# Optimization experiments

Hardware: AMD Instinct MI355X
Metric: run time of the kernel (lower is better)

## Reference

```python
import jax, jax.numpy as jnp
import numpy as np

ROT = 256  # Hadamard block size (ConvLinear4bit._n)


def _hadamard(n):
    # Sylvester construction of the n x n Hadamard matrix (n power of 2)
    H = np.array([[1.0]], dtype=np.float32)
    while H.shape[0] < n:
        H = np.block([[H, H], [H, -H]])
    return jnp.asarray(H / np.sqrt(n), dtype=jnp.float32)


def setup_inputs() -> dict:
    key = jax.random.key(0)
    k1, k2, k3, k4 = jax.random.split(key, 4)
    N, D_in, D_out = 4096, 4096, 4096
    x = jax.random.normal(k1, (N, D_in), dtype=jnp.float32)
    # unpacked int4 weights in [-7, 7] (logical content of the packed uint8 buffer)
    weight_int = jax.random.randint(k2, (D_out, D_in), -7, 8, dtype=jnp.int32)
    # per-output-row weight scales (quarot: max|W_rot| / 7)
    w_scale = jax.random.uniform(k3, (D_out, 1), dtype=jnp.float32) * 0.01 + 1e-4
    bias = jax.random.normal(k4, (D_out,), dtype=jnp.float32) * 0.01
    return {"x": x, "weight_int": weight_int, "w_scale": w_scale, "bias": bias}


def reference(x, weight_int, w_scale, bias):
    N, D = x.shape
    H = _hadamard(ROT)
    # blockwise Hadamard rotation along the feature dim (D is a multiple of ROT)
    x_rot = (x.reshape(N, D // ROT, ROT) @ H).reshape(N, D)
    # per-row symmetric int4 quantization of activations
    scales_x = jnp.max(jnp.abs(x_rot), axis=-1, keepdims=True) / 7.0  # [N, 1]
    q_x = jnp.clip(jnp.round(x_rot / scales_x), -8, 7).astype(jnp.int32)
    acc = jnp.matmul(q_x, weight_int.T)
    # sym_dequant: row scale (activations) * col scale (weights), then bias
    out = acc.astype(jnp.float32) * scales_x * w_scale.T + bias
    return out
```

## Files before the change

### kernel.cpp

```cpp
#include <hip/hip_runtime.h>
#include <math.h>

typedef int v4i  __attribute__((ext_vector_type(4)));
typedef int v16i __attribute__((ext_vector_type(16)));

#define DIM 4096
#define BM 256
#define BK 64
#define ATILE (BM * BK)
#define BUFSZ (2 * ATILE)

__device__ __forceinline__ void async16(const void* g, void* l) {
    __builtin_amdgcn_global_load_lds((__attribute__((address_space(1))) void*)(g),
                                     (__attribute__((address_space(3))) void*)(l),
                                     16, 0, 0);
}

#define VMCNT(N) asm volatile("s_waitcnt vmcnt(" #N ")" ::: "memory")
#define BARRIER() asm volatile("s_barrier" ::: "memory")

__device__ __forceinline__ int swzC(int r) {
    return ((r >> 1) & 3) ^ ((r >> 3) & 3);
}

__global__ __launch_bounds__(256) void prep(const float* __restrict__ x,
                                            const int* __restrict__ w,
                                            signed char* __restrict__ q,
                                            signed char* __restrict__ w8,
                                            float* __restrict__ scales) {
    if (blockIdx.x >= 4096) {
        int i = (blockIdx.x - 4096) * 256 + threadIdx.x;
        int4 v = ((const int4*)w)[i];
        char4 c;
        c.x = (signed char)v.x; c.y = (signed char)v.y;
        c.z = (signed char)v.z; c.w = (signed char)v.w;
        ((char4*)w8)[i] = c;
        return;
    }
    const int row  = blockIdx.x;
    const int lane = threadIdx.x & 63;
    const int wave = threadIdx.x >> 6;
    const float4* xr4 = (const float4*)(x + (size_t)row * DIM);

    float sgn[6];
    #pragma unroll
    for (int i = 0; i < 6; ++i) sgn[i] = (lane & (1 << i)) ? -1.0f : 1.0f;

    float f[4][4];
    #pragma unroll
    for (int b = 0; b < 4; ++b) {
        const int blk = wave + 4 * b;
        float4 v = xr4[blk * 64 + lane];
        float t0 = v.x + v.y, t1 = v.x - v.y;
        float t2 = v.z + v.w, t3 = v.z - v.w;
        f[b][0] = t0 + t2; f[b][1] = t1 + t3;
        f[b][2] = t0 - t2; f[b][3] = t1 - t3;
        #pragma unroll
        for (int st = 0; st < 6; ++st) {
            const int m = 1 << st;
            #pragma unroll
            for (int j = 0; j < 4; ++j) {
                float p = __shfl_xor(f[b][j], m, 64);
                f[b][j] = fmaf(sgn[st], f[b][j], p);
            }
        }
        #pragma unroll
        for (int j = 0; j < 4; ++j) f[b][j] *= 0.0625f;
    }

    float m = 0.0f;
    #pragma unroll
    for (int b = 0; b < 4; ++b)
        #pragma unroll
        for (int j = 0; j < 4; ++j) m = fmaxf(m, fabsf(f[b][j]));
    #pragma unroll
    for (int d = 32; d; d >>= 1) m = fmaxf(m, __shfl_xor(m, d, 64));
    __shared__ float sm[4];
    if (lane == 0) sm[wave] = m;
    __syncthreads();
    m = fmaxf(fmaxf(sm[0], sm[1]), fmaxf(sm[2], sm[3]));

    const float s = m / 7.0f;
    if (threadIdx.x == 0) scales[row] = s;

    char4* qr4 = (char4*)(q + (size_t)row * DIM);
    #pragma unroll
    for (int b = 0; b < 4; ++b) {
        const int blk = wave + 4 * b;
        char4 c;
        int qi;
        qi = (int)rintf(f[b][0] / s); c.x = (signed char)min(7, max(-8, qi));
        qi = (int)rintf(f[b][1] / s); c.y = (signed char)min(7, max(-8, qi));
        qi = (int)rintf(f[b][2] / s); c.z = (signed char)min(7, max(-8, qi));
        qi = (int)rintf(f[b][3] / s); c.w = (signed char)min(7, max(-8, qi));
        qr4[blk * 64 + lane] = c;
    }
}

__global__ __launch_bounds__(512, 2) void gemm_q8(const signed char* __restrict__ A,
                                                  const signed char* __restrict__ B,
                                                  const float* __restrict__ rowScale,
                                                  const float* __restrict__ wscale,
                                                  const float* __restrict__ bias,
                                                  float* __restrict__ out) {
    __shared__ __align__(16) signed char S[4 * BUFSZ];

    const int flat = blockIdx.y * gridDim.x + blockIdx.x;
    const int xcd  = flat & 7;
    const int idx  = flat >> 3;
    const int bm   = ((xcd >> 1) << 2) + (idx & 3);
    const int bn   = ((xcd & 1) << 3) + (idx >> 2);

    const int t = threadIdx.x;
    const int lane = t & 63;
    const int wave = t >> 6;
    const int wm = (wave >> 2) * 128;
    const int wn = (wave & 3) * 64;
    const int l31 = lane & 31, lh = lane >> 5;

    const signed char* ga[2];
    const signed char* gb[2];
    int ldsA[2], ldsB[2];
    #pragma unroll
    for (int h = 0; h < 2; ++h) {
        const int cidx = t + 512 * h;
        const int row  = cidx >> 2;
        const int g    = (cidx & 3) ^ swzC(row);
        ga[h] = A + (size_t)(bm * BM + row) * DIM + g * 16;
        gb[h] = B + (size_t)(bn * BM + row) * DIM + g * 16;
        ldsA[h] = cidx * 16;
        ldsB[h] = ATILE + cidx * 16;
    }

    int offA[4][2], offB[2][2];
    #pragma unroll
    for (int i = 0; i < 4; ++i)
        #pragma unroll
        for (int s = 0; s < 2; ++s) {
            const int r = wm + i * 32 + l31;
            offA[i][s] = r * BK + (((2 * s + lh) ^ swzC(r)) * 16);
        }
    #pragma unroll
    for (int j = 0; j < 2; ++j)
        #pragma unroll
        for (int s = 0; s < 2; ++s) {
            const int c = wn + j * 32 + l31;
            offB[j][s] = ATILE + c * BK + (((2 * s + lh) ^ swzC(c)) * 16);
        }

    v16i acc[4][2] = {};

#define STAGE(P) do {                                                          \
        async16(ga[0], &S[(P) * BUFSZ + ldsA[0]]); ga[0] += BK;                \
        async16(ga[1], &S[(P) * BUFSZ + ldsA[1]]); ga[1] += BK;                \
        async16(gb[0], &S[(P) * BUFSZ + ldsB[0]]); gb[0] += BK;                \
        async16(gb[1], &S[(P) * BUFSZ + ldsB[1]]); gb[1] += BK;                \
    } while (0)

#define COMPUTE(P) do {                                                        \
        __builtin_amdgcn_s_setprio(1);                                         \
        _Pragma("unroll")                                                      \
        for (int s = 0; s < 2; ++s) {                                          \
            const v4i a0 = *(const v4i*)&S[(P) * BUFSZ + offA[0][s]];          \
            const v4i a1 = *(const v4i*)&S[(P) * BUFSZ + offA[1][s]];          \
            const v4i a2 = *(const v4i*)&S[(P) * BUFSZ + offA[2][s]];          \
            const v4i a3 = *(const v4i*)&S[(P) * BUFSZ + offA[3][s]];          \
            const v4i b0 = *(const v4i*)&S[(P) * BUFSZ + offB[0][s]];          \
            const v4i b1 = *(const v4i*)&S[(P) * BUFSZ + offB[1][s]];          \
            acc[0][0] = __builtin_amdgcn_mfma_i32_32x32x32_i8(a0, b0, acc[0][0], 0, 0, 0); \
            acc[0][1] = __builtin_amdgcn_mfma_i32_32x32x32_i8(a0, b1, acc[0][1], 0, 0, 0); \
            acc[1][0] = __builtin_amdgcn_mfma_i32_32x32x32_i8(a1, b0, acc[1][0], 0, 0, 0); \
            acc[1][1] = __builtin_amdgcn_mfma_i32_32x32x32_i8(a1, b1, acc[1][1], 0, 0, 0); \
            acc[2][0] = __builtin_amdgcn_mfma_i32_32x32x32_i8(a2, b0, acc[2][0], 0, 0, 0); \
            acc[2][1] = __builtin_amdgcn_mfma_i32_32x32x32_i8(a2, b1, acc[2][1], 0, 0, 0); \
            acc[3][0] = __builtin_amdgcn_mfma_i32_32x32x32_i8(a3, b0, acc[3][0], 0, 0, 0); \
            acc[3][1] = __builtin_amdgcn_mfma_i32_32x32x32_i8(a3, b1, acc[3][1], 0, 0, 0); \
        }                                                                      \
        __builtin_amdgcn_s_setprio(0);                                         \
    } while (0)

    STAGE(0); STAGE(1); STAGE(2);
    #pragma unroll 1
    for (int it = 0; it < 15; ++it) {
        VMCNT(8); BARRIER(); STAGE(3); COMPUTE(0);
        VMCNT(8); BARRIER(); STAGE(0); COMPUTE(1);
        VMCNT(8); BARRIER(); STAGE(1); COMPUTE(2);
        VMCNT(8); BARRIER(); STAGE(2); COMPUTE(3);
    }
    VMCNT(8); BARRIER(); STAGE(3); COMPUTE(0);
    VMCNT(8); BARRIER();           COMPUTE(1);
    VMCNT(4); BARRIER();           COMPUTE(2);
    VMCNT(0); BARRIER();           COMPUTE(3);

#undef STAGE
#undef COMPUTE

    #pragma unroll
    for (int j = 0; j < 2; ++j) {
        const int col = bn * BM + wn + j * 32 + l31;
        const float ws = wscale[col];
        const float bs = bias[col];
        #pragma unroll
        for (int i = 0; i < 4; ++i) {
            const int rb = bm * BM + wm + i * 32 + 4 * lh;
            #pragma unroll
            for (int r = 0; r < 16; ++r) {
                const int row = rb + (r & 3) + 8 * (r >> 2);
                out[(size_t)row * DIM + col] =
                    ((float)acc[i][j][r] * rowScale[row]) * ws + bs;
            }
        }
    }
}

extern "C" void kernel_launch(void* const* d_in, const int* in_sizes, int n_in,
                              void* d_out, int out_size, void* d_ws, size_t ws_size,
                              hipStream_t stream) {
    const float* x      = (const float*)d_in[0];
    const int*   wint   = (const int*)d_in[1];
    const float* wscale = (const float*)d_in[2];
    const float* bias   = (const float*)d_in[3];
    float* out = (float*)d_out;

    signed char* q8 = (signed char*)d_ws;
    signed char* w8 = q8 + (size_t)DIM * DIM;
    float* sx = (float*)(w8 + (size_t)DIM * DIM);

    prep<<<4096 + 16384, 256, 0, stream>>>(x, wint, q8, w8, sx);
    gemm_q8<<<dim3(DIM / BM, DIM / BM), 512, 0, stream>>>(q8, w8, sx, wscale, bias, out);
}
```

Before: 243.5 us.

## Double BK to 128 with two-stage LDS pipeline and 8-way XOR swizzle

```diff
diff --git a/kernel.cpp b/kernel.cpp
--- a/kernel.cpp
+++ b/kernel.cpp
@@ -6,7 +6,7 @@
 
 #define DIM 4096
 #define BM 256
-#define BK 64
+#define BK 128
 #define ATILE (BM * BK)
 #define BUFSZ (2 * ATILE)
 
@@ -18,10 +18,6 @@
 
 #define VMCNT(N) asm volatile("s_waitcnt vmcnt(" #N ")" ::: "memory")
 #define BARRIER() asm volatile("s_barrier" ::: "memory")
-
-__device__ __forceinline__ int swzC(int r) {
-    return ((r >> 1) & 3) ^ ((r >> 3) & 3);
-}
 
 __global__ __launch_bounds__(256) void prep(const float* __restrict__ x,
                                             const int* __restrict__ w,
@@ -64,8 +60,6 @@
                 f[b][j] = fmaf(sgn[st], f[b][j], p);
             }
         }
-        #pragma unroll
-        for (int j = 0; j < 4; ++j) f[b][j] *= 0.0625f;
     }
 
     float m = 0.0f;
@@ -80,8 +74,9 @@
     __syncthreads();
     m = fmaxf(fmaxf(sm[0], sm[1]), fmaxf(sm[2], sm[3]));
 
-    const float s = m / 7.0f;
+    const float s = (m * 0.0625f) / 7.0f;
     if (threadIdx.x == 0) scales[row] = s;
+    const float rinv = 7.0f / m;
 
     char4* qr4 = (char4*)(q + (size_t)row * DIM);
     #pragma unroll
@@ -89,10 +84,10 @@
         const int blk = wave + 4 * b;
         char4 c;
         int qi;
-        qi = (int)rintf(f[b][0] / s); c.x = (signed char)min(7, max(-8, qi));
-        qi = (int)rintf(f[b][1] / s); c.y = (signed char)min(7, max(-8, qi));
-        qi = (int)rintf(f[b][2] / s); c.z = (signed char)min(7, max(-8, qi));
-        qi = (int)rintf(f[b][3] / s); c.w = (signed char)min(7, max(-8, qi));
+        qi = (int)rintf(f[b][0] * rinv); c.x = (signed char)min(7, max(-8, qi));
+        qi = (int)rintf(f[b][1] * rinv); c.y = (signed char)min(7, max(-8, qi));
+        qi = (int)rintf(f[b][2] * rinv); c.z = (signed char)min(7, max(-8, qi));
+        qi = (int)rintf(f[b][3] * rinv); c.w = (signed char)min(7, max(-8, qi));
         qr4[blk * 64 + lane] = c;
     }
 }
@@ -103,7 +98,7 @@
                                                   const float* __restrict__ wscale,
                                                   const float* __restrict__ bias,
                                                   float* __restrict__ out) {
-    __shared__ __align__(16) signed char S[4 * BUFSZ];
+    __shared__ __align__(16) signed char S[2 * BUFSZ];
 
     const int flat = blockIdx.y * gridDim.x + blockIdx.x;
     const int xcd  = flat & 7;
@@ -118,49 +113,50 @@
     const int wn = (wave & 3) * 64;
     const int l31 = lane & 31, lh = lane >> 5;
 
-    const signed char* ga[2];
-    const signed char* gb[2];
-    int ldsA[2], ldsB[2];
-    #pragma unroll
-    for (int h = 0; h < 2; ++h) {
+    const signed char* ga[4];
+    const signed char* gb[4];
+    int ldsA[4], ldsB[4];
+    #pragma unroll
+    for (int h = 0; h < 4; ++h) {
         const int cidx = t + 512 * h;
-        const int row  = cidx >> 2;
-        const int g    = (cidx & 3) ^ swzC(row);
+        const int row  = cidx >> 3;
+        const int g    = (cidx & 7) ^ (row & 7);
         ga[h] = A + (size_t)(bm * BM + row) * DIM + g * 16;
         gb[h] = B + (size_t)(bn * BM + row) * DIM + g * 16;
         ldsA[h] = cidx * 16;
         ldsB[h] = ATILE + cidx * 16;
     }
 
-    int offA[4][2], offB[2][2];
+    int offA[4][4], offB[2][4];
     #pragma unroll
     for (int i = 0; i < 4; ++i)
         #pragma unroll
-        for (int s = 0; s < 2; ++s) {
+        for (int s = 0; s < 4; ++s) {
             const int r = wm + i * 32 + l31;
-            offA[i][s] = r * BK + (((2 * s + lh) ^ swzC(r)) * 16);
+            offA[i][s] = r * BK + (((2 * s + lh) ^ (r & 7)) * 16);
         }
     #pragma unroll
     for (int j = 0; j < 2; ++j)
         #pragma unroll
-        for (int s = 0; s < 2; ++s) {
+        for (int s = 0; s < 4; ++s) {
             const int c = wn + j * 32 + l31;
-            offB[j][s] = ATILE + c * BK + (((2 * s + lh) ^ swzC(c)) * 16);
+            offB[j][s] = ATILE + c * BK + (((2 * s + lh) ^ (c & 7)) * 16);
         }
 
     v16i acc[4][2] = {};
 
 #define STAGE(P) do {                                                          \
-        async16(ga[0], &S[(P) * BUFSZ + ldsA[0]]); ga[0] += BK;                \
-        async16(ga[1], &S[(P) * BUFSZ + ldsA[1]]); ga[1] += BK;                \
-        async16(gb[0], &S[(P) * BUFSZ + ldsB[0]]); gb[0] += BK;                \
-        async16(gb[1], &S[(P) * BUFSZ + ldsB[1]]); gb[1] += BK;                \
+        _Pragma("unroll")                                                      \
+        for (int h = 0; h < 4; ++h) {                                          \
+            async16(ga[h], &S[(P) * BUFSZ + ldsA[h]]); ga[h] += BK;            \
+            async16(gb[h], &S[(P) * BUFSZ + ldsB[h]]); gb[h] += BK;            \
+        }                                                                      \
     } while (0)
 
 #define COMPUTE(P) do {                                                        \
         __builtin_amdgcn_s_setprio(1);                                         \
         _Pragma("unroll")                                                      \
-        for (int s = 0; s < 2; ++s) {                                          \
+        for (int s = 0; s < 4; ++s) {                                          \
             const v4i a0 = *(const v4i*)&S[(P) * BUFSZ + offA[0][s]];          \
             const v4i a1 = *(const v4i*)&S[(P) * BUFSZ + offA[1][s]];          \
             const v4i a2 = *(const v4i*)&S[(P) * BUFSZ + offA[2][s]];          \
@@ -179,18 +175,14 @@
         __builtin_amdgcn_s_setprio(0);                                         \
     } while (0)
 
-    STAGE(0); STAGE(1); STAGE(2);
+    STAGE(0);
     #pragma unroll 1
     for (int it = 0; it < 15; ++it) {
-        VMCNT(8); BARRIER(); STAGE(3); COMPUTE(0);
-        VMCNT(8); BARRIER(); STAGE(0); COMPUTE(1);
-        VMCNT(8); BARRIER(); STAGE(1); COMPUTE(2);
-        VMCNT(8); BARRIER(); STAGE(2); COMPUTE(3);
-    }
-    VMCNT(8); BARRIER(); STAGE(3); COMPUTE(0);
-    VMCNT(8); BARRIER();           COMPUTE(1);
-    VMCNT(4); BARRIER();           COMPUTE(2);
-    VMCNT(0); BARRIER();           COMPUTE(3);
+        STAGE(1); VMCNT(8); BARRIER(); COMPUTE(0); BARRIER();
+        STAGE(0); VMCNT(8); BARRIER(); COMPUTE(1); BARRIER();
+    }
+    STAGE(1); VMCNT(8); BARRIER(); COMPUTE(0); BARRIER();
+    VMCNT(0); BARRIER(); COMPUTE(1);
 
 #undef STAGE
 #undef COMPUTE
```

After: 266.3 us. 1.09x slower.

## Pre-arrange LDS tiles in MFMA fragment order and prefetch next-stage fragments

Applied to the files above, without the earlier changes.

```diff
diff --git a/kernel.cpp b/kernel.cpp
--- a/kernel.cpp
+++ b/kernel.cpp
@@ -18,10 +18,6 @@
 
 #define VMCNT(N) asm volatile("s_waitcnt vmcnt(" #N ")" ::: "memory")
 #define BARRIER() asm volatile("s_barrier" ::: "memory")
-
-__device__ __forceinline__ int swzC(int r) {
-    return ((r >> 1) & 3) ^ ((r >> 3) & 3);
-}
 
 __global__ __launch_bounds__(256) void prep(const float* __restrict__ x,
                                             const int* __restrict__ w,
@@ -64,8 +60,6 @@
                 f[b][j] = fmaf(sgn[st], f[b][j], p);
             }
         }
-        #pragma unroll
-        for (int j = 0; j < 4; ++j) f[b][j] *= 0.0625f;
     }
 
     float m = 0.0f;
@@ -80,8 +74,9 @@
     __syncthreads();
     m = fmaxf(fmaxf(sm[0], sm[1]), fmaxf(sm[2], sm[3]));
 
-    const float s = m / 7.0f;
+    const float s = (m * 0.0625f) / 7.0f;
     if (threadIdx.x == 0) scales[row] = s;
+    const float rinv = 7.0f / m;
 
     char4* qr4 = (char4*)(q + (size_t)row * DIM);
     #pragma unroll
@@ -89,10 +84,10 @@
         const int blk = wave + 4 * b;
         char4 c;
         int qi;
-        qi = (int)rintf(f[b][0] / s); c.x = (signed char)min(7, max(-8, qi));
-        qi = (int)rintf(f[b][1] / s); c.y = (signed char)min(7, max(-8, qi));
-        qi = (int)rintf(f[b][2] / s); c.z = (signed char)min(7, max(-8, qi));
-        qi = (int)rintf(f[b][3] / s); c.w = (signed char)min(7, max(-8, qi));
+        qi = (int)rintf(f[b][0] * rinv); c.x = (signed char)min(7, max(-8, qi));
+        qi = (int)rintf(f[b][1] * rinv); c.y = (signed char)min(7, max(-8, qi));
+        qi = (int)rintf(f[b][2] * rinv); c.z = (signed char)min(7, max(-8, qi));
+        qi = (int)rintf(f[b][3] * rinv); c.w = (signed char)min(7, max(-8, qi));
         qr4[blk * 64 + lane] = c;
     }
 }
@@ -124,31 +119,24 @@
     #pragma unroll
     for (int h = 0; h < 2; ++h) {
         const int cidx = t + 512 * h;
-        const int row  = cidx >> 2;
-        const int g    = (cidx & 3) ^ swzC(row);
-        ga[h] = A + (size_t)(bm * BM + row) * DIM + g * 16;
-        gb[h] = B + (size_t)(bn * BM + row) * DIM + g * 16;
+        const int b    = cidx >> 6;
+        const int g    = b >> 1;
+        const int sH   = b & 1;
+        const int l    = cidx & 63;
+        const int row  = g * 32 + (l & 31);
+        const int kb   = sH * 32 + (l >> 5) * 16;
+        ga[h] = A + (size_t)(bm * BM + row) * DIM + kb;
+        gb[h] = B + (size_t)(bn * BM + row) * DIM + kb;
         ldsA[h] = cidx * 16;
         ldsB[h] = ATILE + cidx * 16;
     }
 
-    int offA[4][2], offB[2][2];
-    #pragma unroll
-    for (int i = 0; i < 4; ++i)
-        #pragma unroll
-        for (int s = 0; s < 2; ++s) {
-            const int r = wm + i * 32 + l31;
-            offA[i][s] = r * BK + (((2 * s + lh) ^ swzC(r)) * 16);
-        }
-    #pragma unroll
-    for (int j = 0; j < 2; ++j)
-        #pragma unroll
-        for (int s = 0; s < 2; ++s) {
-            const int c = wn + j * 32 + l31;
-            offB[j][s] = ATILE + c * BK + (((2 * s + lh) ^ swzC(c)) * 16);
-        }
+    const signed char* rbA = &S[(wave >> 2) * 8192 + lane * 16];
+    const signed char* rbB = &S[ATILE + (wave & 3) * 4096 + lane * 16];
 
     v16i acc[4][2] = {};
+    v4i fa0[4], fb0[2];
+    v4i fa1[4], fb1[2];
 
 #define STAGE(P) do {                                                          \
         async16(ga[0], &S[(P) * BUFSZ + ldsA[0]]); ga[0] += BK;                \
@@ -157,43 +145,77 @@
         async16(gb[1], &S[(P) * BUFSZ + ldsB[1]]); gb[1] += BK;                \
     } while (0)
 
-#define COMPUTE(P) do {                                                        \
+#define RD_S0(P) do {                                                          \
+        fa0[0] = *(const v4i*)(rbA + (P) * BUFSZ + 0 * 2048);                  \
+        fa0[1] = *(const v4i*)(rbA + (P) * BUFSZ + 1 * 2048);                  \
+        fa0[2] = *(const v4i*)(rbA + (P) * BUFSZ + 2 * 2048);                  \
+        fa0[3] = *(const v4i*)(rbA + (P) * BUFSZ + 3 * 2048);                  \
+        fb0[0] = *(const v4i*)(rbB + (P) * BUFSZ + 0 * 2048);                  \
+        fb0[1] = *(const v4i*)(rbB + (P) * BUFSZ + 1 * 2048);                  \
+    } while (0)
+
+#define RD_S1(P) do {                                                          \
+        fa1[0] = *(const v4i*)(rbA + (P) * BUFSZ + 0 * 2048 + 1024);           \
+        fa1[1] = *(const v4i*)(rbA + (P) * BUFSZ + 1 * 2048 + 1024);           \
+        fa1[2] = *(const v4i*)(rbA + (P) * BUFSZ + 2 * 2048 + 1024);           \
+        fa1[3] = *(const v4i*)(rbA + (P) * BUFSZ + 3 * 2048 + 1024);           \
+        fb1[0] = *(const v4i*)(rbB + (P) * BUFSZ + 0 * 2048 + 1024);           \
+        fb1[1] = *(const v4i*)(rbB + (P) * BUFSZ + 1 * 2048 + 1024);           \
+    } while (0)
+
+#define MFMA8(FA, FB) do {                                                     \
         __builtin_amdgcn_s_setprio(1);                                         \
-        _Pragma("unroll")                                                      \
-        for (int s = 0; s < 2; ++s) {                                          \
-            const v4i a0 = *(const v4i*)&S[(P) * BUFSZ + offA[0][s]];          \
-            const v4i a1 = *(const v4i*)&S[(P) * BUFSZ + offA[1][s]];          \
-            const v4i a2 = *(const v4i*)&S[(P) * BUFSZ + offA[2][s]];          \
-            const v4i a3 = *(const v4i*)&S[(P) * BUFSZ + offA[3][s]];          \
-            const v4i b0 = *(const v4i*)&S[(P) * BUFSZ + offB[0][s]];          \
-            const v4i b1 = *(const v4i*)&S[(P) * BUFSZ + offB[1][s]];          \
-            acc[0][0] = __builtin_amdgcn_mfma_i32_32x32x32_i8(a0, b0, acc[0][0], 0, 0, 0); \
-            acc[0][1] = __builtin_amdgcn_mfma_i32_32x32x32_i8(a0, b1, acc[0][1], 0, 0, 0); \
-            acc[1][0] = __builtin_amdgcn_mfma_i32_32x32x32_i8(a1, b0, acc[1][0], 0, 0, 0); \
-            acc[1][1] = __builtin_amdgcn_mfma_i32_32x32x32_i8(a1, b1, acc[1][1], 0, 0, 0); \
-            acc[2][0] = __builtin_amdgcn_mfma_i32_32x32x32_i8(a2, b0, acc[2][0], 0, 0, 0); \
-            acc[2][1] = __builtin_amdgcn_mfma_i32_32x32x32_i8(a2, b1, acc[2][1], 0, 0, 0); \
-            acc[3][0] = __builtin_amdgcn_mfma_i32_32x32x32_i8(a3, b0, acc[3][0], 0, 0, 0); \
-            acc[3][1] = __builtin_amdgcn_mfma_i32_32x32x32_i8(a3, b1, acc[3][1], 0, 0, 0); \
-        }                                                                      \
+        acc[0][0] = __builtin_amdgcn_mfma_i32_32x32x32_i8(FA[0], FB[0], acc[0][0], 0, 0, 0); \
+        acc[0][1] = __builtin_amdgcn_mfma_i32_32x32x32_i8(FA[0], FB[1], acc[0][1], 0, 0, 0); \
+        acc[1][0] = __builtin_amdgcn_mfma_i32_32x32x32_i8(FA[1], FB[0], acc[1][0], 0, 0, 0); \
+        acc[1][1] = __builtin_amdgcn_mfma_i32_32x32x32_i8(FA[1], FB[1], acc[1][1], 0, 0, 0); \
+        acc[2][0] = __builtin_amdgcn_mfma_i32_32x32x32_i8(FA[2], FB[0], acc[2][0], 0, 0, 0); \
+        acc[2][1] = __builtin_amdgcn_mfma_i32_32x32x32_i8(FA[2], FB[1], acc[2][1], 0, 0, 0); \
+        acc[3][0] = __builtin_amdgcn_mfma_i32_32x32x32_i8(FA[3], FB[0], acc[3][0], 0, 0, 0); \
+        acc[3][1] = __builtin_amdgcn_mfma_i32_32x32x32_i8(FA[3], FB[1], acc[3][1], 0, 0, 0); \
         __builtin_amdgcn_s_setprio(0);                                         \
     } while (0)
 
+#define SUBSTEP(P, PN, SP, VN) do {                                            \
+        VMCNT(VN); BARRIER();             \
+        STAGE(SP);                                                             \
+        RD_S1(P);                                \
+        MFMA8(fa0, fb0);                 \
+        RD_S0(PN);                     \
+        MFMA8(fa1, fb1);                                     \
+    } while (0)
+
+#define SUBSTEP_NS(P, PN, VN) do {                                             \
+        VMCNT(VN); BARRIER();                                                  \
+        RD_S1(P);                                                              \
+        MFMA8(fa0, fb0);                                                       \
+        RD_S0(PN);                                                             \
+        MFMA8(fa1, fb1);                                                       \
+    } while (0)
+
     STAGE(0); STAGE(1); STAGE(2);
+    VMCNT(8); BARRIER();
+    RD_S0(0);
     #pragma unroll 1
     for (int it = 0; it < 15; ++it) {
-        VMCNT(8); BARRIER(); STAGE(3); COMPUTE(0);
-        VMCNT(8); BARRIER(); STAGE(0); COMPUTE(1);
-        VMCNT(8); BARRIER(); STAGE(1); COMPUTE(2);
-        VMCNT(8); BARRIER(); STAGE(2); COMPUTE(3);
-    }
-    VMCNT(8); BARRIER(); STAGE(3); COMPUTE(0);
-    VMCNT(8); BARRIER();           COMPUTE(1);
-    VMCNT(4); BARRIER();           COMPUTE(2);
-    VMCNT(0); BARRIER();           COMPUTE(3);
-
+        SUBSTEP(0, 1, 3, 4);
+        SUBSTEP(1, 2, 0, 4);
+        SUBSTEP(2, 3, 1, 4);
+        SUBSTEP(3, 0, 2, 4);
+    }
+    SUBSTEP(0, 1, 3, 4);
+    SUBSTEP_NS(1, 2, 4);
+    SUBSTEP_NS(2, 3, 0);
+    RD_S1(3);
+    MFMA8(fa0, fb0);
+    MFMA8(fa1, fb1);
+
+#undef SUBSTEP
+#undef SUBSTEP_NS
 #undef STAGE
-#undef COMPUTE
+#undef RD_S0
+#undef RD_S1
+#undef MFMA8
 
     #pragma unroll
     for (int j = 0; j < 2; ++j) {
```

Measured after the change: 251.6 us. 3.3% more time.
